# Optimization experiments

Measured on AMD Instinct MI355X. Metric: run time of the kernel, lower is better.

## Reference

```python
import jax, jax.numpy as jnp
import numpy as np


def setup_inputs() -> dict:
    key = jax.random.key(0)
    ks = jax.random.split(key, 6)
    B, C, H, W = 8, 512, 64, 64
    s = 1.0 / np.sqrt(C)
    return {
        "x": jax.random.normal(ks[0], (B, C, H, W), dtype=jnp.float32),
        "w_phi": jax.random.normal(ks[1], (C, C), dtype=jnp.float32) * s,
        "w_theta": jax.random.normal(ks[2], (C, C), dtype=jnp.float32) * s,
        "w_g": jax.random.normal(ks[3], (C, C), dtype=jnp.float32) * s,
        "w_mask": jax.random.normal(ks[4], (C, C), dtype=jnp.float32) * s,
        "gamma": jax.random.normal(ks[5], (1,), dtype=jnp.float32) * 0.1,
    }


def reference(x, w_phi, w_theta, w_g, w_mask, gamma):
    b, c, h, w = x.shape
    n = h * w
    xf = x.reshape(b, c, n)  # flatten spatial: [b, c, n]
    # 1x1 convs (bias=False) are channel-mixing GEMMs
    phi = jnp.einsum("oc,bcn->bon", w_phi, xf)    # [b, c, n]
    theta = jnp.einsum("oc,bcn->bon", w_theta, xf)  # [b, c, n]
    g = jnp.einsum("oc,bcn->bon", w_g, xf)        # [b, c, n]
    # channel-channel attention (unscaled), softmax over last dim
    attn = jax.nn.softmax(jnp.einsum("bcn,bdn->bcd", phi, theta), axis=-1)  # [b, c, c]
    y = jnp.einsum("bcd,bdn->bcn", attn, g)  # [b, c, n]
    # faithful to torch: permute(0,2,1).contiguous().view(b, c, h, w)
    y = jnp.transpose(y, (0, 2, 1)).reshape(b, c, h, w)
    mask = jnp.einsum("oc,bchw->bohw", w_mask, y)
    return mask * gamma[0] + x
```

## Files before the change

kernel.cpp:

```cpp
#include <hip/hip_runtime.h>
#include <hip/hip_bf16.h>

constexpr int BATCH = 8;
constexpr int C = 512;
constexpr int HW = 4096;
constexpr long CN = (long)C * HW;
constexpr long CC = (long)C * C;

typedef __attribute__((ext_vector_type(8))) short short8;
typedef __attribute__((ext_vector_type(4))) short bf16x4;
typedef __attribute__((ext_vector_type(4))) float f32x4;

__device__ __forceinline__ void gload16(const void* g, void* l) {
  __builtin_amdgcn_global_load_lds(
      (const __attribute__((address_space(1))) void*)g,
      (__attribute__((address_space(3))) void*)l, 16, 0, 0);
}

__device__ __forceinline__ void hilo(float v, __hip_bfloat16& h, __hip_bfloat16& l) {
  h = __float2bfloat16(v);
  l = __float2bfloat16(v - __bfloat162float(h));
}
__device__ __forceinline__ short bfs(float v) {
  __hip_bfloat16 h = __float2bfloat16(v);
  return *(short*)&h;
}

__device__ __forceinline__ int cidx32(int r, int ch) {
  return ((r >> 1) * 8 + ((((r & 1) << 2) | ch) ^ ((r >> 1) & 7))) * 8;
}
__device__ __forceinline__ void sdec32(int s, int& r, int& ch) {
  int R = s >> 3, q = s & 7, v = q ^ (R & 7);
  r = (R << 1) | (v >> 2);
  ch = v & 3;
}

#define WAIT_VM(n) asm volatile("s_waitcnt vmcnt(" #n ")" ::: "memory")

__global__ __launch_bounds__(256) void convx_k(
    const float* __restrict__ x, __hip_bfloat16* __restrict__ xhi,
    __hip_bfloat16* __restrict__ xt) {
  const int b = blockIdx.z;
  const int n0 = blockIdx.x * 64, c0 = blockIdx.y * 64;
  const float* xb = x + (long)b * CN;
  __shared__ short t[64 * 65];
  const int tid = threadIdx.x;
#pragma unroll
  for (int it = 0; it < 2; ++it) {
    int slot = it * 256 + tid;
    int r = slot >> 3, cc = (slot & 7) * 8;
    const float* src = xb + (long)(c0 + r) * HW + n0 + cc;
    f32x4 v0 = *(const f32x4*)src, v1 = *(const f32x4*)(src + 4);
    short8 hh;
#pragma unroll
    for (int e = 0; e < 4; ++e) {
      hh[e] = bfs(v0[e]);
      hh[4 + e] = bfs(v1[e]);
    }
    long idx = (long)b * CN + (long)(c0 + r) * HW + n0 + cc;
    *(short8*)((short*)xhi + idx) = hh;
#pragma unroll
    for (int e = 0; e < 8; ++e) t[r * 65 + cc + e] = hh[e];
  }
  __syncthreads();
#pragma unroll
  for (int it = 0; it < 2; ++it) {
    int slot = it * 256 + tid;
    int r = slot >> 3, cc = (slot & 7) * 8;
    short8 o;
#pragma unroll
    for (int e = 0; e < 8; ++e) o[e] = t[(cc + e) * 65 + r];
    *(short8*)((short*)xt + (long)b * CN + (long)(n0 + r) * C + c0 + cc) = o;
  }
}

__global__ __launch_bounds__(256) void wprep_k(
    const float* __restrict__ wphi, const float* __restrict__ wtheta,
    const float* __restrict__ wg, const float* __restrict__ wmask,
    __hip_bfloat16* __restrict__ wph, __hip_bfloat16* __restrict__ wpl,
    __hip_bfloat16* __restrict__ wth, __hip_bfloat16* __restrict__ wtl,
    __hip_bfloat16* __restrict__ wgT, __hip_bfloat16* __restrict__ wm16) {
  const int z = blockIdx.z;
  const int r0 = blockIdx.y * 64, c0 = blockIdx.x * 64;
  const int tid = threadIdx.x;
  if (z == 2) {
    __shared__ __hip_bfloat16 t[64][65];
#pragma unroll
    for (int i = 0; i < 16; ++i) {
      int e = i * 256 + tid;
      int r = e >> 6, c = e & 63;
      t[r][c] = __float2bfloat16(wg[(long)(r0 + r) * C + c0 + c]);
    }
    __syncthreads();
#pragma unroll
    for (int i = 0; i < 16; ++i) {
      int e = i * 256 + tid;
      int r = e >> 6, c = e & 63;
      wgT[(long)(c0 + r) * C + r0 + c] = t[c][r];
    }
  } else {
#pragma unroll
    for (int i = 0; i < 16; ++i) {
      int e = i * 256 + tid;
      int r = e >> 6, c = e & 63;
      long idx = (long)(r0 + r) * C + c0 + c;
      if (z == 0) {
        __hip_bfloat16 h, l;
        hilo(wphi[idx], h, l);
        wph[idx] = h; wpl[idx] = l;
      } else if (z == 1) {
        __hip_bfloat16 h, l;
        hilo(wtheta[idx], h, l);
        wth[idx] = h; wtl[idx] = l;
      } else {
        wm16[idx] = __float2bfloat16(wmask[idx]);
      }
    }
  }
}

__global__ __launch_bounds__(256) void gram_k(
    const __hip_bfloat16* __restrict__ xhi, float* __restrict__ gpart) {
  const int b = blockIdx.z;
  const int ks = blockIdx.y;
  int i = 0, rem0 = blockIdx.x;
  while (rem0 >= 4 - i) { rem0 -= 4 - i; ++i; }
  const int j = i + rem0;
  const int m0 = i * 128, n0 = j * 128;

  const short* X = (const short*)(xhi + (long)b * CN);
  __shared__ short lds[4 * 8192];
  const int tid = threadIdx.x, w = tid >> 6, lane = tid & 63;

  f32x4 acc[4][4] = {};
  const int wr = (w >> 1) * 64, wc = (w & 1) * 64;
  const int kbeg = ks * 1024;
  constexpr int NST = 32;

  auto STAGE = [&](int buf, int k0) {
    short* lb = lds + buf * 8192;
#pragma unroll
    for (int it = 0; it < 4; ++it) {
      int s = (w & 1) * 256 + it * 64 + lane;
      int r, ch;
      sdec32(s, r, ch);
      int gr = (w < 2) ? (m0 + r) : (n0 + r);
      gload16(X + (long)gr * HW + k0 + ch * 8, lb + (w >> 1) * 4096 + s * 8);
    }
  };

  const int chf = lane >> 4, rl = lane & 15;
  int aoff[4], boff[4];
#pragma unroll
  for (int mi = 0; mi < 4; ++mi) aoff[mi] = cidx32(wr + mi * 16 + rl, chf);
#pragma unroll
  for (int ni = 0; ni < 4; ++ni) boff[ni] = 4096 + cidx32(wc + ni * 16 + rl, chf);

  STAGE(0, kbeg);
  STAGE(1, kbeg + 32);
  STAGE(2, kbeg + 64);

#pragma unroll
  for (int t = 0; t < NST; ++t) {
    if (t + 3 < NST) STAGE((t + 3) & 3, kbeg + (t + 3) * 32);
    const int rm = NST - 1 - t;
    if (rm >= 3) WAIT_VM(12);
    else if (rm == 2) WAIT_VM(8);
    else if (rm == 1) WAIT_VM(4);
    else WAIT_VM(0);
    __builtin_amdgcn_s_barrier();
    const short* lb = lds + (t & 3) * 8192;
    short8 af[4], bfr[4];
#pragma unroll
    for (int mi = 0; mi < 4; ++mi) af[mi] = *(const short8*)(lb + aoff[mi]);
#pragma unroll
    for (int ni = 0; ni < 4; ++ni) bfr[ni] = *(const short8*)(lb + boff[ni]);
#pragma unroll
    for (int mi = 0; mi < 4; ++mi)
#pragma unroll
      for (int ni = 0; ni < 4; ++ni)
        acc[mi][ni] = __builtin_amdgcn_mfma_f32_16x16x32_bf16(af[mi], bfr[ni], acc[mi][ni], 0, 0, 0);
    __builtin_amdgcn_s_barrier();
  }

  float* P = gpart + ((((long)b * 10 + blockIdx.x) * 4 + ks) << 14);
#pragma unroll
  for (int mi = 0; mi < 4; ++mi)
#pragma unroll
    for (int ni = 0; ni < 4; ++ni)
#pragma unroll
      for (int rr = 0; rr < 4; ++rr) {
        int row = wr + mi * 16 + (lane >> 4) * 4 + rr;
        int col = wc + ni * 16 + (lane & 15);
        P[row * 128 + col] = acc[mi][ni][rr];
      }
}

__global__ __launch_bounds__(256) void gred_k(
    const float* __restrict__ gpart, __hip_bfloat16* __restrict__ gh,
    __hip_bfloat16* __restrict__ gl) {
  const int b = blockIdx.z;
  const int half = blockIdx.y;
  int i = 0, rem = blockIdx.x;
  while (rem >= 4 - i) { rem -= 4 - i; ++i; }
  const int j = i + rem;
  const int m0 = i * 128, n0 = j * 128;
  const float* P = gpart + (((long)b * 10 + blockIdx.x) << 16) + half * 8192;
  __shared__ float T[128][65];
  const int tid = threadIdx.x;
  const long dbase = (long)b * CC;

#pragma unroll
  for (int q = 0; q < 8; ++q) {
    int e = q * 1024 + tid * 4;
    int r = e >> 7, c = e & 127;
    f32x4 s = {};
#pragma unroll
    for (int ks = 0; ks < 4; ++ks) s += *(const f32x4*)(P + (ks << 14) + e);
    bf16x4 hh, ll;
#pragma unroll
    for (int u = 0; u < 4; ++u) {
      __hip_bfloat16 h, l;
      hilo(s[u], h, l);
      hh[u] = *(short*)&h;
      ll[u] = *(short*)&l;
      T[c + u][r] = s[u];
    }
    long idx = dbase + (long)(m0 + half * 64 + r) * 512 + n0 + c;
    *(bf16x4*)((short*)gh + idx) = hh;
    *(bf16x4*)((short*)gl + idx) = ll;
  }
  if (i != j) {
    __syncthreads();
#pragma unroll
    for (int q = 0; q < 8; ++q) {
      int e = q * 1024 + tid * 4;
      int rp = e >> 6, cp = e & 63;
      bf16x4 hh, ll;
#pragma unroll
      for (int u = 0; u < 4; ++u) {
        __hip_bfloat16 h, l;
        hilo(T[rp][cp + u], h, l);
        hh[u] = *(short*)&h;
        ll[u] = *(short*)&l;
      }
      long idx = dbase + (long)(n0 + rp) * 512 + m0 + half * 64 + cp;
      *(bf16x4*)((short*)gh + idx) = hh;
      *(bf16x4*)((short*)gl + idx) = ll;
    }
  }
}

template <int AH, int BH, int EPI>
__global__ __launch_bounds__(256) void nt_small(
    const __hip_bfloat16* __restrict__ Ah_, const __hip_bfloat16* __restrict__ Al_,
    const __hip_bfloat16* __restrict__ Bh_, const __hip_bfloat16* __restrict__ Bl_,
    long aStr, long bStr, void* __restrict__ out1, void* __restrict__ out2) {
  const int b = blockIdx.z;
  const int m0 = blockIdx.y * 64, n0 = blockIdx.x * 64;
  const short* Ahp = (const short*)(Ah_ + (long)b * aStr);
  const short* Alp = AH ? (const short*)(Al_ + (long)b * aStr) : nullptr;
  const short* Bhp = (const short*)(Bh_ + (long)b * bStr);
  const short* Blp = BH ? (const short*)(Bl_ + (long)b * bStr) : nullptr;
  constexpr int PAN = (AH && BH) ? 4 : 2;
  __shared__ short lds[2 * PAN * 4096];
  const int tid = threadIdx.x, w = tid >> 6, lane = tid & 63;

  f32x4 acc[2][2] = {};
  const int wr = (w >> 1) * 32, wc = (w & 1) * 32;

  auto STAGE = [&](int buf, int k0) {
    short* lb = lds + buf * PAN * 4096;
    if constexpr (AH && BH) {
      const short* src = (w == 0) ? Ahp : (w == 1) ? Alp : (w == 2) ? Bhp : Blp;
      const int rowbase = (w & 2) ? n0 : m0;
      short* lt = lb + w * 4096;
#pragma unroll
      for (int it = 0; it < 8; ++it) {
        int slot = it * 64 + lane;
        int r = slot >> 3, p = slot & 7, c = p ^ (r & 7);
        gload16(src + (long)(rowbase + r) * 512 + k0 + c * 8, lt + slot * 8);
      }
    } else {
      const short* src = (w < 2) ? Ahp : Bhp;
      const int rowbase = (w < 2) ? m0 : n0;
      short* lt = lb + (w >> 1) * 4096;
#pragma unroll
      for (int it = 0; it < 4; ++it) {
        int slot = (w & 1) * 256 + it * 64 + lane;
        int r = slot >> 3, p = slot & 7, c = p ^ (r & 7);
        gload16(src + (long)(rowbase + r) * 512 + k0 + c * 8, lt + slot * 8);
      }
    }
  };

  STAGE(0, 0);
  asm volatile("s_waitcnt vmcnt(0)" ::: "memory");
  __builtin_amdgcn_s_barrier();

  for (int t = 0; t < 8; ++t) {
    if (t < 7) STAGE((t + 1) & 1, (t + 1) * 64);
    const short* lb = lds + (t & 1) * PAN * 4096;
#pragma unroll
    for (int kh = 0; kh < 2; ++kh) {
      short8 ah[2], al[2], bh[2], bl[2];
      const int ch = kh * 4 + (lane >> 4);
#pragma unroll
      for (int mi = 0; mi < 2; ++mi) {
        int r = wr + mi * 16 + (lane & 15);
        int off = (r * 8 + (ch ^ (r & 7))) * 8;
        ah[mi] = *(const short8*)(lb + off);
        if constexpr (AH) al[mi] = *(const short8*)(lb + 4096 + off);
      }
#pragma unroll
      for (int ni = 0; ni < 2; ++ni) {
        int r = wc + ni * 16 + (lane & 15);
        int off = (r * 8 + (ch ^ (r & 7))) * 8;
        bh[ni] = *(const short8*)(lb + ((AH && BH) ? 8192 : 4096) + off);
        if constexpr (BH) bl[ni] = *(const short8*)(lb + 12288 + off);
      }
#pragma unroll
      for (int mi = 0; mi < 2; ++mi)
#pragma unroll
        for (int ni = 0; ni < 2; ++ni) {
          acc[mi][ni] = __builtin_amdgcn_mfma_f32_16x16x32_bf16(ah[mi], bh[ni], acc[mi][ni], 0, 0, 0);
          if constexpr (BH)
            acc[mi][ni] = __builtin_amdgcn_mfma_f32_16x16x32_bf16(ah[mi], bl[ni], acc[mi][ni], 0, 0, 0);
          if constexpr (AH)
            acc[mi][ni] = __builtin_amdgcn_mfma_f32_16x16x32_bf16(al[mi], bh[ni], acc[mi][ni], 0, 0, 0);
        }
    }
    asm volatile("s_waitcnt vmcnt(0)" ::: "memory");
    __builtin_amdgcn_s_barrier();
  }

#pragma unroll
  for (int mi = 0; mi < 2; ++mi)
#pragma unroll
    for (int ni = 0; ni < 2; ++ni)
#pragma unroll
      for (int rr = 0; rr < 4; ++rr) {
        int row = m0 + wr + mi * 16 + (lane >> 4) * 4 + rr;
        int col = n0 + wc + ni * 16 + (lane & 15);
        long idx = (long)b * CC + (long)row * 512 + col;
        float v = acc[mi][ni][rr];
        if constexpr (EPI == 0) {
          __hip_bfloat16 h, l;
          hilo(v, h, l);
          ((__hip_bfloat16*)out1)[idx] = h;
          ((__hip_bfloat16*)out2)[idx] = l;
        } else if constexpr (EPI == 1) {
          ((float*)out1)[idx] = v;
        } else {
          ((__hip_bfloat16*)out1)[idx] = __float2bfloat16(v);
        }
      }
}

__global__ __launch_bounds__(256) void softmax_k(const float* __restrict__ a,
                                                 __hip_bfloat16* __restrict__ o) {
  const float* row = a + (long)blockIdx.x * 512;
  __hip_bfloat16* orow = o + (long)blockIdx.x * 512;
  const int t = threadIdx.x;
  float v0 = row[t], v1 = row[t + 256];
  __shared__ float sm[256];
  sm[t] = fmaxf(v0, v1);
  __syncthreads();
  for (int s = 128; s > 0; s >>= 1) {
    if (t < s) sm[t] = fmaxf(sm[t], sm[t + s]);
    __syncthreads();
  }
  float mx = sm[0];
  __syncthreads();
  float e0 = expf(v0 - mx), e1 = expf(v1 - mx);
  sm[t] = e0 + e1;
  __syncthreads();
  for (int s = 128; s > 0; s >>= 1) {
    if (t < s) sm[t] += sm[t + s];
    __syncthreads();
  }
  float inv = 1.0f / sm[0];
  orow[t] = __float2bfloat16(e0 * inv);
  orow[t + 256] = __float2bfloat16(e1 * inv);
}

template <int MODE>
__global__ __launch_bounds__(256) void big_k(
    const __hip_bfloat16* __restrict__ Aw, const __hip_bfloat16* __restrict__ Bm,
    void* __restrict__ Cout, const float* __restrict__ x,
    const float* __restrict__ gammaPtr, long aStride) {
  const int b = blockIdx.z;
  const int lin = ((blockIdx.x & 7) << 4) | (blockIdx.x >> 3);
  const int m0 = (lin & 3) * 128;
  const int n0 = (lin >> 2) * 128;
  const short* A = (const short*)(Aw + (long)b * aStride);
  const short* B = (const short*)(Bm + (long)b * CN);
  __shared__ short lds[4 * 8192];
  const int tid = threadIdx.x, w = tid >> 6, lane = tid & 63;

  f32x4 acc[4][4] = {};
  const int wr = (w >> 1) * 64, wc = (w & 1) * 64;
  constexpr int NST = 16;

  auto STAGE = [&](int buf, int k0) {
    short* lb = lds + buf * 8192;
#pragma unroll
    for (int it = 0; it < 4; ++it) {
      int s = (w & 1) * 256 + it * 64 + lane;
      int r, ch;
      sdec32(s, r, ch);
      if (w < 2) {
        gload16(A + (long)(m0 + r) * 512 + k0 + ch * 8, lb + s * 8);
      } else {
        int gr = (MODE == 0) ? (n0 + (r & 15) * 8 + (r >> 4)) : (n0 + r);
        gload16(B + (long)gr * 512 + k0 + ch * 8, lb + 4096 + s * 8);
      }
    }
  };

  const int chf = lane >> 4, rl = lane & 15;
  int aoff[4], boff[4];
#pragma unroll
  for (int mi = 0; mi < 4; ++mi) aoff[mi] = cidx32(wr + mi * 16 + rl, chf);
#pragma unroll
  for (int ni = 0; ni < 4; ++ni) boff[ni] = 4096 + cidx32(wc + ni * 16 + rl, chf);

  STAGE(0, 0);
  STAGE(1, 32);
  STAGE(2, 64);

#pragma unroll
  for (int t = 0; t < NST; ++t) {
    if (t + 3 < NST) STAGE((t + 3) & 3, (t + 3) * 32);
    const int rm = NST - 1 - t;
    if (rm >= 3) WAIT_VM(12);
    else if (rm == 2) WAIT_VM(8);
    else if (rm == 1) WAIT_VM(4);
    else WAIT_VM(0);
    __builtin_amdgcn_s_barrier();
    const short* lb = lds + (t & 3) * 8192;
    short8 af[4], bfr[4];
#pragma unroll
    for (int mi = 0; mi < 4; ++mi) af[mi] = *(const short8*)(lb + aoff[mi]);
#pragma unroll
    for (int ni = 0; ni < 4; ++ni) bfr[ni] = *(const short8*)(lb + boff[ni]);
#pragma unroll
    for (int mi = 0; mi < 4; ++mi)
#pragma unroll
      for (int ni = 0; ni < 4; ++ni)
        acc[mi][ni] = __builtin_amdgcn_mfma_f32_16x16x32_bf16(af[mi], bfr[ni], acc[mi][ni], 0, 0, 0);
    __builtin_amdgcn_s_barrier();
  }

  if (MODE == 0) {
    __hip_bfloat16* yv = (__hip_bfloat16*)Cout + (long)b * CN;
    const int u = lane & 15;
#pragma unroll
    for (int mi = 0; mi < 4; ++mi)
#pragma unroll
      for (int ni = 0; ni < 4; ++ni) {
        int t = (wc >> 4) + ni;
        long base = ((long)(t * 512 + m0 + wr + mi * 16 + (lane >> 4) * 4)) * 512 +
                    (n0 >> 3) + u;
#pragma unroll
        for (int r = 0; r < 4; ++r)
          yv[base + (long)r * 512] = __float2bfloat16(acc[mi][ni][r]);
      }
  } else {
    float* outp = (float*)Cout + (long)b * CN;
    const float* xb = x + (long)b * CN;
    const float g0 = gammaPtr[0];
#pragma unroll
    for (int mi = 0; mi < 4; ++mi)
#pragma unroll
      for (int ni = 0; ni < 4; ++ni)
#pragma unroll
        for (int r = 0; r < 4; ++r) {
          long idx = (long)(m0 + wr + mi * 16 + (lane >> 4) * 4 + r) * HW +
                     n0 + wc + ni * 16 + (lane & 15);
          outp[idx] = g0 * acc[mi][ni][r] + xb[idx];
        }
  }
}

extern "C" void kernel_launch(void* const* d_in, const int* in_sizes, int n_in,
                              void* d_out, int out_size, void* d_ws, size_t ws_size,
                              hipStream_t stream) {
  const float* x       = (const float*)d_in[0];
  const float* w_phi   = (const float*)d_in[1];
  const float* w_theta = (const float*)d_in[2];
  const float* w_g     = (const float*)d_in[3];
  const float* w_mask  = (const float*)d_in[4];
  const float* gamma   = (const float*)d_in[5];
  float* out = (float*)d_out;

  __hip_bfloat16* xhi = (__hip_bfloat16*)d_ws;
  __hip_bfloat16* xt  = xhi + BATCH * CN;
  __hip_bfloat16* gh  = xt + BATCH * CN;
  __hip_bfloat16* gl  = gh + BATCH * CC;
  __hip_bfloat16* t1h = gl + BATCH * CC;
  __hip_bfloat16* t1l = t1h + BATCH * CC;
  __hip_bfloat16* wph = t1l + BATCH * CC;
  __hip_bfloat16* wpl = wph + CC;
  __hip_bfloat16* wth = wpl + CC;
  __hip_bfloat16* wtl = wth + CC;
  __hip_bfloat16* wgT = wtl + CC;
  __hip_bfloat16* wm16 = wgT + CC;
  float* gpart = (float*)(wm16 + CC);
  float* logits           = (float*)gh;
  __hip_bfloat16* attn16  = t1h;
  __hip_bfloat16* mb16    = t1l;
  __hip_bfloat16* yvT     = xhi;

  convx_k<<<dim3(64, 8, BATCH), 256, 0, stream>>>(x, xhi, xt);
  wprep_k<<<dim3(8, 8, 4), 256, 0, stream>>>(w_phi, w_theta, w_g, w_mask,
                                             wph, wpl, wth, wtl, wgT, wm16);
  gram_k<<<dim3(10, 4, BATCH), 256, 0, stream>>>(xhi, gpart);
  gred_k<<<dim3(10, 2, BATCH), 256, 0, stream>>>(gpart, gh, gl);
  nt_small<1, 1, 0><<<dim3(8, 8, BATCH), 256, 0, stream>>>(
      wph, wpl, gh, gl, 0, CC, t1h, t1l);
  nt_small<1, 1, 1><<<dim3(8, 8, BATCH), 256, 0, stream>>>(
      t1h, t1l, wth, wtl, CC, 0, logits, nullptr);
  softmax_k<<<dim3(BATCH * C), dim3(256), 0, stream>>>(logits, attn16);
  nt_small<0, 0, 2><<<dim3(8, 8, BATCH), 256, 0, stream>>>(
      attn16, nullptr, wgT, nullptr, CC, 0, mb16, nullptr);
  big_k<0><<<dim3(128, 1, BATCH), 256, 0, stream>>>(mb16, xt, yvT, nullptr, nullptr, CC);
  big_k<1><<<dim3(128, 1, BATCH), 256, 0, stream>>>(wm16, yvT, out, x, gamma, 0);
}
```

Before: 270.4 us.

## Fuse small attention GEMM chain and softmax into one per-row-block kernel

Replaces the three nt_small launches and the separate softmax kernel with one chain_k kernel. Each block computes 32 rows of W_phi·G, keeps the intermediate in LDS as hi/lo bf16, multiplies by W_theta, does the softmax in registers with cross-wave reductions, then multiplies by W_g^T and writes mb16. This removes global round trips for t1, the logits and attn, plus three launches. The cost is a grid of only 128 blocks reading B operands straight from global memory without LDS staging, which may leave the GPU underused. It also remaps gram_k block indices so the batch index varies fastest across consecutive blocks.

```diff
diff --git a/kernel.cpp b/kernel.cpp
--- a/kernel.cpp
+++ b/kernel.cpp
@@ -121,9 +121,12 @@
 
 __global__ __launch_bounds__(256) void gram_k(
     const __hip_bfloat16* __restrict__ xhi, float* __restrict__ gpart) {
-  const int b = blockIdx.z;
-  const int ks = blockIdx.y;
-  int i = 0, rem0 = blockIdx.x;
+  const int f = blockIdx.x + 10 * (blockIdx.y + 4 * blockIdx.z);
+  const int b = f & 7;
+  const int rdec = f >> 3;
+  const int ks = rdec / 10;
+  const int tile = rdec % 10;
+  int i = 0, rem0 = tile;
   while (rem0 >= 4 - i) { rem0 -= 4 - i; ++i; }
   const int j = i + rem0;
   const int m0 = i * 128, n0 = j * 128;
@@ -145,7 +148,8 @@
       int r, ch;
       sdec32(s, r, ch);
       int gr = (w < 2) ? (m0 + r) : (n0 + r);
-      gload16(X + (long)gr * HW + k0 + ch * 8, lb + (w >> 1) * 4096 + s * 8);
+      gload16(X + (long)gr * HW + k0 + ch * 8, lds + (buf * 8192 + (w >> 1) * 4096 + s * 8));
+      (void)lb;
     }
   };
 
@@ -183,7 +187,7 @@
     __builtin_amdgcn_s_barrier();
   }
 
-  float* P = gpart + ((((long)b * 10 + blockIdx.x) * 4 + ks) << 14);
+  float* P = gpart + ((((long)b * 10 + tile) * 4 + ks) << 14);
 #pragma unroll
   for (int mi = 0; mi < 4; ++mi)
 #pragma unroll
@@ -251,137 +255,208 @@
   }
 }
 
-template <int AH, int BH, int EPI>
-__global__ __launch_bounds__(256) void nt_small(
-    const __hip_bfloat16* __restrict__ Ah_, const __hip_bfloat16* __restrict__ Al_,
-    const __hip_bfloat16* __restrict__ Bh_, const __hip_bfloat16* __restrict__ Bl_,
-    long aStr, long bStr, void* __restrict__ out1, void* __restrict__ out2) {
-  const int b = blockIdx.z;
-  const int m0 = blockIdx.y * 64, n0 = blockIdx.x * 64;
-  const short* Ahp = (const short*)(Ah_ + (long)b * aStr);
-  const short* Alp = AH ? (const short*)(Al_ + (long)b * aStr) : nullptr;
-  const short* Bhp = (const short*)(Bh_ + (long)b * bStr);
-  const short* Blp = BH ? (const short*)(Bl_ + (long)b * bStr) : nullptr;
-  constexpr int PAN = (AH && BH) ? 4 : 2;
-  __shared__ short lds[2 * PAN * 4096];
+__global__ __launch_bounds__(256) void chain_k(
+    const __hip_bfloat16* __restrict__ wph_, const __hip_bfloat16* __restrict__ wpl_,
+    const __hip_bfloat16* __restrict__ gh_, const __hip_bfloat16* __restrict__ gl_,
+    const __hip_bfloat16* __restrict__ wth_, const __hip_bfloat16* __restrict__ wtl_,
+    const __hip_bfloat16* __restrict__ wgT_, __hip_bfloat16* __restrict__ mb16) {
+  const int f = blockIdx.x + 16 * blockIdx.z;
+  const int b = f & 7;
+  const int m0 = (f >> 3) * 32;
+
+  const short* Ah = (const short*)wph_;
+  const short* Al = (const short*)wpl_;
+  const short* Gh = (const short*)(gh_ + (long)b * CC);
+  const short* Gl = (const short*)(gl_ + (long)b * CC);
+  const short* Th = (const short*)wth_;
+  const short* Tl = (const short*)wtl_;
+  const short* Wg = (const short*)wgT_;
+
+  __shared__ short t1h[32 * 512];
+  __shared__ short t1l[32 * 512];
+  __shared__ short at[32 * 512];
+  __shared__ float red[4][32];
+  __shared__ float rowv[32];
+
   const int tid = threadIdx.x, w = tid >> 6, lane = tid & 63;
-
-  f32x4 acc[2][2] = {};
-  const int wr = (w >> 1) * 32, wc = (w & 1) * 32;
-
-  auto STAGE = [&](int buf, int k0) {
-    short* lb = lds + buf * PAN * 4096;
-    if constexpr (AH && BH) {
-      const short* src = (w == 0) ? Ahp : (w == 1) ? Alp : (w == 2) ? Bhp : Blp;
-      const int rowbase = (w & 2) ? n0 : m0;
-      short* lt = lb + w * 4096;
-#pragma unroll
-      for (int it = 0; it < 8; ++it) {
-        int slot = it * 64 + lane;
-        int r = slot >> 3, p = slot & 7, c = p ^ (r & 7);
-        gload16(src + (long)(rowbase + r) * 512 + k0 + c * 8, lt + slot * 8);
-      }
-    } else {
-      const short* src = (w < 2) ? Ahp : Bhp;
-      const int rowbase = (w < 2) ? m0 : n0;
-      short* lt = lb + (w >> 1) * 4096;
-#pragma unroll
-      for (int it = 0; it < 4; ++it) {
-        int slot = (w & 1) * 256 + it * 64 + lane;
-        int r = slot >> 3, p = slot & 7, c = p ^ (r & 7);
-        gload16(src + (long)(rowbase + r) * 512 + k0 + c * 8, lt + slot * 8);
-      }
-    }
-  };
-
-  STAGE(0, 0);
-  asm volatile("s_waitcnt vmcnt(0)" ::: "memory");
-  __builtin_amdgcn_s_barrier();
-
-  for (int t = 0; t < 8; ++t) {
-    if (t < 7) STAGE((t + 1) & 1, (t + 1) * 64);
-    const short* lb = lds + (t & 1) * PAN * 4096;
-#pragma unroll
-    for (int kh = 0; kh < 2; ++kh) {
-      short8 ah[2], al[2], bh[2], bl[2];
-      const int ch = kh * 4 + (lane >> 4);
+  const int ch = lane >> 4, u = lane & 15;
+  const int nbase = w * 128;
+
+  f32x4 acc[2][8];
+
+#pragma unroll
+  for (int mi = 0; mi < 2; ++mi)
+#pragma unroll
+    for (int ni = 0; ni < 8; ++ni) acc[mi][ni] = (f32x4){0.f, 0.f, 0.f, 0.f};
+
+#pragma unroll 2
+  for (int kb = 0; kb < 512; kb += 32) {
+    short8 ah[2], al[2];
+#pragma unroll
+    for (int mi = 0; mi < 2; ++mi) {
+      int ao = (m0 + mi * 16 + u) * 512 + kb + ch * 8;
+      ah[mi] = *(const short8*)(Ah + ao);
+      al[mi] = *(const short8*)(Al + ao);
+    }
+#pragma unroll
+    for (int ni = 0; ni < 8; ++ni) {
+      int bo = (nbase + ni * 16 + u) * 512 + kb + ch * 8;
+      short8 bh = *(const short8*)(Gh + bo);
+      short8 bl = *(const short8*)(Gl + bo);
 #pragma unroll
       for (int mi = 0; mi < 2; ++mi) {
-        int r = wr + mi * 16 + (lane & 15);
-        int off = (r * 8 + (ch ^ (r & 7))) * 8;
-        ah[mi] = *(const short8*)(lb + off);
-        if constexpr (AH) al[mi] = *(const short8*)(lb + 4096 + off);
-      }
-#pragma unroll
-      for (int ni = 0; ni < 2; ++ni) {
-        int r = wc + ni * 16 + (lane & 15);
-        int off = (r * 8 + (ch ^ (r & 7))) * 8;
-        bh[ni] = *(const short8*)(lb + ((AH && BH) ? 8192 : 4096) + off);
-        if constexpr (BH) bl[ni] = *(const short8*)(lb + 12288 + off);
-      }
+        acc[mi][ni] = __builtin_amdgcn_mfma_f32_16x16x32_bf16(ah[mi], bh, acc[mi][ni], 0, 0, 0);
+        acc[mi][ni] = __builtin_amdgcn_mfma_f32_16x16x32_bf16(ah[mi], bl, acc[mi][ni], 0, 0, 0);
+        acc[mi][ni] = __builtin_amdgcn_mfma_f32_16x16x32_bf16(al[mi], bh, acc[mi][ni], 0, 0, 0);
+      }
+    }
+  }
+
+#pragma unroll
+  for (int mi = 0; mi < 2; ++mi)
+#pragma unroll
+    for (int ni = 0; ni < 8; ++ni)
+#pragma unroll
+      for (int rr = 0; rr < 4; ++rr) {
+        int m = mi * 16 + ch * 4 + rr;
+        int c = nbase + ni * 16 + u;
+        int addr = m * 512 + ((((c >> 3) ^ (m & 7)) << 3) | (c & 7));
+        __hip_bfloat16 h, l;
+        hilo(acc[mi][ni][rr], h, l);
+        t1h[addr] = *(short*)&h;
+        t1l[addr] = *(short*)&l;
+      }
+  __syncthreads();
+
+#pragma unroll
+  for (int mi = 0; mi < 2; ++mi)
+#pragma unroll
+    for (int ni = 0; ni < 8; ++ni) acc[mi][ni] = (f32x4){0.f, 0.f, 0.f, 0.f};
+
+#pragma unroll 2
+  for (int kb = 0; kb < 512; kb += 32) {
+    short8 ah[2], al[2];
+#pragma unroll
+    for (int mi = 0; mi < 2; ++mi) {
+      int m = mi * 16 + u;
+      int p = (kb >> 3) + ch;
+      int off = (m * 64 + (p ^ (m & 7))) * 8;
+      ah[mi] = *(const short8*)(t1h + off);
+      al[mi] = *(const short8*)(t1l + off);
+    }
+#pragma unroll
+    for (int ni = 0; ni < 8; ++ni) {
+      int bo = (nbase + ni * 16 + u) * 512 + kb + ch * 8;
+      short8 bh = *(const short8*)(Th + bo);
+      short8 bl = *(const short8*)(Tl + bo);
+#pragma unroll
+      for (int mi = 0; mi < 2; ++mi) {
+        acc[mi][ni] = __builtin_amdgcn_mfma_f32_16x16x32_bf16(ah[mi], bh, acc[mi][ni], 0, 0, 0);
+        acc[mi][ni] = __builtin_amdgcn_mfma_f32_16x16x32_bf16(ah[mi], bl, acc[mi][ni], 0, 0, 0);
+        acc[mi][ni] = __builtin_amdgcn_mfma_f32_16x16x32_bf16(al[mi], bh, acc[mi][ni], 0, 0, 0);
+      }
+    }
+  }
+
+  float rm[2][4];
+#pragma unroll
+  for (int mi = 0; mi < 2; ++mi)
+#pragma unroll
+    for (int rr = 0; rr < 4; ++rr) {
+      float v = acc[mi][0][rr];
+#pragma unroll
+      for (int ni = 1; ni < 8; ++ni) v = fmaxf(v, acc[mi][ni][rr]);
+#pragma unroll
+      for (int s = 1; s < 16; s <<= 1) v = fmaxf(v, __shfl_xor(v, s));
+      rm[mi][rr] = v;
+    }
+  if (u == 0)
+#pragma unroll
+    for (int mi = 0; mi < 2; ++mi)
+#pragma unroll
+      for (int rr = 0; rr < 4; ++rr) red[w][mi * 16 + ch * 4 + rr] = rm[mi][rr];
+  __syncthreads();
+  if (tid < 32)
+    rowv[tid] = fmaxf(fmaxf(red[0][tid], red[1][tid]), fmaxf(red[2][tid], red[3][tid]));
+  __syncthreads();
+
+  float rs[2][4];
+#pragma unroll
+  for (int mi = 0; mi < 2; ++mi)
+#pragma unroll
+    for (int rr = 0; rr < 4; ++rr) {
+      float M = rowv[mi * 16 + ch * 4 + rr];
+      float s = 0.f;
+#pragma unroll
+      for (int ni = 0; ni < 8; ++ni) {
+        float e = expf(acc[mi][ni][rr] - M);
+        acc[mi][ni][rr] = e;
+        s += e;
+      }
+#pragma unroll
+      for (int t = 1; t < 16; t <<= 1) s += __shfl_xor(s, t);
+      rs[mi][rr] = s;
+    }
+  if (u == 0)
+#pragma unroll
+    for (int mi = 0; mi < 2; ++mi)
+#pragma unroll
+      for (int rr = 0; rr < 4; ++rr) red[w][mi * 16 + ch * 4 + rr] = rs[mi][rr];
+  __syncthreads();
+  if (tid < 32)
+    rowv[tid] = 1.0f / (red[0][tid] + red[1][tid] + red[2][tid] + red[3][tid]);
+  __syncthreads();
+
+#pragma unroll
+  for (int mi = 0; mi < 2; ++mi)
+#pragma unroll
+    for (int rr = 0; rr < 4; ++rr) {
+      int m = mi * 16 + ch * 4 + rr;
+      float inv = rowv[m];
+#pragma unroll
+      for (int ni = 0; ni < 8; ++ni) {
+        int c = nbase + ni * 16 + u;
+        int addr = m * 512 + ((((c >> 3) ^ (m & 7)) << 3) | (c & 7));
+        at[addr] = bfs(acc[mi][ni][rr] * inv);
+      }
+    }
+  __syncthreads();
+
+#pragma unroll
+  for (int mi = 0; mi < 2; ++mi)
+#pragma unroll
+    for (int ni = 0; ni < 8; ++ni) acc[mi][ni] = (f32x4){0.f, 0.f, 0.f, 0.f};
+
+#pragma unroll 2
+  for (int kb = 0; kb < 512; kb += 32) {
+    short8 ah[2];
+#pragma unroll
+    for (int mi = 0; mi < 2; ++mi) {
+      int m = mi * 16 + u;
+      int p = (kb >> 3) + ch;
+      ah[mi] = *(const short8*)(at + (m * 64 + (p ^ (m & 7))) * 8);
+    }
+#pragma unroll
+    for (int ni = 0; ni < 8; ++ni) {
+      int bo = (nbase + ni * 16 + u) * 512 + kb + ch * 8;
+      short8 bg = *(const short8*)(Wg + bo);
 #pragma unroll
       for (int mi = 0; mi < 2; ++mi)
-#pragma unroll
-        for (int ni = 0; ni < 2; ++ni) {
-          acc[mi][ni] = __builtin_amdgcn_mfma_f32_16x16x32_bf16(ah[mi], bh[ni], acc[mi][ni], 0, 0, 0);
-          if constexpr (BH)
-            acc[mi][ni] = __builtin_amdgcn_mfma_f32_16x16x32_bf16(ah[mi], bl[ni], acc[mi][ni], 0, 0, 0);
-          if constexpr (AH)
-            acc[mi][ni] = __builtin_amdgcn_mfma_f32_16x16x32_bf16(al[mi], bh[ni], acc[mi][ni], 0, 0, 0);
-        }
-    }
-    asm volatile("s_waitcnt vmcnt(0)" ::: "memory");
-    __builtin_amdgcn_s_barrier();
-  }
-
-#pragma unroll
-  for (int mi = 0; mi < 2; ++mi)
-#pragma unroll
-    for (int ni = 0; ni < 2; ++ni)
+        acc[mi][ni] = __builtin_amdgcn_mfma_f32_16x16x32_bf16(ah[mi], bg, acc[mi][ni], 0, 0, 0);
+    }
+  }
+
+  short* outp = (short*)mb16 + (long)b * CC;
+#pragma unroll
+  for (int mi = 0; mi < 2; ++mi)
+#pragma unroll
+    for (int ni = 0; ni < 8; ++ni)
 #pragma unroll
       for (int rr = 0; rr < 4; ++rr) {
-        int row = m0 + wr + mi * 16 + (lane >> 4) * 4 + rr;
-        int col = n0 + wc + ni * 16 + (lane & 15);
-        long idx = (long)b * CC + (long)row * 512 + col;
-        float v = acc[mi][ni][rr];
-        if constexpr (EPI == 0) {
-          __hip_bfloat16 h, l;
-          hilo(v, h, l);
-          ((__hip_bfloat16*)out1)[idx] = h;
-          ((__hip_bfloat16*)out2)[idx] = l;
-        } else if constexpr (EPI == 1) {
-          ((float*)out1)[idx] = v;
-        } else {
-          ((__hip_bfloat16*)out1)[idx] = __float2bfloat16(v);
-        }
-      }
-}
-
-__global__ __launch_bounds__(256) void softmax_k(const float* __restrict__ a,
-                                                 __hip_bfloat16* __restrict__ o) {
-  const float* row = a + (long)blockIdx.x * 512;
-  __hip_bfloat16* orow = o + (long)blockIdx.x * 512;
-  const int t = threadIdx.x;
-  float v0 = row[t], v1 = row[t + 256];
-  __shared__ float sm[256];
-  sm[t] = fmaxf(v0, v1);
-  __syncthreads();
-  for (int s = 128; s > 0; s >>= 1) {
-    if (t < s) sm[t] = fmaxf(sm[t], sm[t + s]);
-    __syncthreads();
-  }
-  float mx = sm[0];
-  __syncthreads();
-  float e0 = expf(v0 - mx), e1 = expf(v1 - mx);
-  sm[t] = e0 + e1;
-  __syncthreads();
-  for (int s = 128; s > 0; s >>= 1) {
-    if (t < s) sm[t] += sm[t + s];
-    __syncthreads();
-  }
-  float inv = 1.0f / sm[0];
-  orow[t] = __float2bfloat16(e0 * inv);
-  orow[t + 256] = __float2bfloat16(e1 * inv);
+        int row = m0 + mi * 16 + ch * 4 + rr;
+        int col = nbase + ni * 16 + u;
+        outp[row * 512 + col] = bfs(acc[mi][ni][rr]);
+      }
 }
 
 template <int MODE>
@@ -507,23 +582,17 @@
   __hip_bfloat16* wgT = wtl + CC;
   __hip_bfloat16* wm16 = wgT + CC;
   float* gpart = (float*)(wm16 + CC);
-  float* logits           = (float*)gh;
-  __hip_bfloat16* attn16  = t1h;
   __hip_bfloat16* mb16    = t1l;
   __hip_bfloat16* yvT     = xhi;
+  (void)t1h;
 
   convx_k<<<dim3(64, 8, BATCH), 256, 0, stream>>>(x, xhi, xt);
   wprep_k<<<dim3(8, 8, 4), 256, 0, stream>>>(w_phi, w_theta, w_g, w_mask,
                                              wph, wpl, wth, wtl, wgT, wm16);
   gram_k<<<dim3(10, 4, BATCH), 256, 0, stream>>>(xhi, gpart);
   gred_k<<<dim3(10, 2, BATCH), 256, 0, stream>>>(gpart, gh, gl);
-  nt_small<1, 1, 0><<<dim3(8, 8, BATCH), 256, 0, stream>>>(
-      wph, wpl, gh, gl, 0, CC, t1h, t1l);
-  nt_small<1, 1, 1><<<dim3(8, 8, BATCH), 256, 0, stream>>>(
-      t1h, t1l, wth, wtl, CC, 0, logits, nullptr);
-  softmax_k<<<dim3(BATCH * C), dim3(256), 0, stream>>>(logits, attn16);
-  nt_small<0, 0, 2><<<dim3(8, 8, BATCH), 256, 0, stream>>>(
-      attn16, nullptr, wgT, nullptr, CC, 0, mb16, nullptr);
+  chain_k<<<dim3(16, 1, BATCH), 256, 0, stream>>>(wph, wpl, gh, gl,
+                                                  wth, wtl, wgT, mb16);
   big_k<0><<<dim3(128, 1, BATCH), 256, 0, stream>>>(mb16, xt, yvT, nullptr, nullptr, CC);
   big_k<1><<<dim3(128, 1, BATCH), 256, 0, stream>>>(wm16, yvT, out, x, gamma, 0);
 }
```

After: 328.7 us. 21.6% more time.

## Interleave batch in block index for small kernels and use wave-per-row softmax

Applied to the files above, without the earlier changes.

Block indices for gram, gram-reduce and the small NT GEMMs are flattened so batch is the fastest-varying index. Consecutive workgroups then come from different batches, which changes how work spreads across XCDs and caches. The softmax is rewritten so each wavefront handles one row using vector loads and shuffle reductions, replacing a shared-memory tree with many barriers. The remapping may lower L2 locality within a batch on some chiplets.

```diff
diff --git a/kernel.cpp b/kernel.cpp
--- a/kernel.cpp
+++ b/kernel.cpp
@@ -121,9 +121,12 @@
 
 __global__ __launch_bounds__(256) void gram_k(
     const __hip_bfloat16* __restrict__ xhi, float* __restrict__ gpart) {
-  const int b = blockIdx.z;
-  const int ks = blockIdx.y;
-  int i = 0, rem0 = blockIdx.x;
+  const int f = blockIdx.x + 10 * (blockIdx.y + 4 * blockIdx.z);
+  const int b = f & 7;
+  const int rdec = f >> 3;
+  const int ks = rdec / 10;
+  const int tile = rdec % 10;
+  int i = 0, rem0 = tile;
   while (rem0 >= 4 - i) { rem0 -= 4 - i; ++i; }
   const int j = i + rem0;
   const int m0 = i * 128, n0 = j * 128;
@@ -138,14 +141,13 @@
   constexpr int NST = 32;
 
   auto STAGE = [&](int buf, int k0) {
-    short* lb = lds + buf * 8192;
 #pragma unroll
     for (int it = 0; it < 4; ++it) {
       int s = (w & 1) * 256 + it * 64 + lane;
       int r, ch;
       sdec32(s, r, ch);
       int gr = (w < 2) ? (m0 + r) : (n0 + r);
-      gload16(X + (long)gr * HW + k0 + ch * 8, lb + (w >> 1) * 4096 + s * 8);
+      gload16(X + (long)gr * HW + k0 + ch * 8, lds + (buf * 8192 + (w >> 1) * 4096 + s * 8));
     }
   };
 
@@ -183,7 +185,7 @@
     __builtin_amdgcn_s_barrier();
   }
 
-  float* P = gpart + ((((long)b * 10 + blockIdx.x) * 4 + ks) << 14);
+  float* P = gpart + ((((long)b * 10 + tile) * 4 + ks) << 14);
 #pragma unroll
   for (int mi = 0; mi < 4; ++mi)
 #pragma unroll
@@ -199,13 +201,16 @@
 __global__ __launch_bounds__(256) void gred_k(
     const float* __restrict__ gpart, __hip_bfloat16* __restrict__ gh,
     __hip_bfloat16* __restrict__ gl) {
-  const int b = blockIdx.z;
-  const int half = blockIdx.y;
-  int i = 0, rem = blockIdx.x;
+  const int id = blockIdx.x;
+  const int b = id & 7;
+  const int t2 = id >> 3;
+  const int tile = t2 % 10;
+  const int half = t2 / 10;
+  int i = 0, rem = tile;
   while (rem >= 4 - i) { rem -= 4 - i; ++i; }
   const int j = i + rem;
   const int m0 = i * 128, n0 = j * 128;
-  const float* P = gpart + (((long)b * 10 + blockIdx.x) << 16) + half * 8192;
+  const float* P = gpart + (((long)b * 10 + tile) << 16) + half * 8192;
   __shared__ float T[128][65];
   const int tid = threadIdx.x;
   const long dbase = (long)b * CC;
@@ -256,8 +261,10 @@
     const __hip_bfloat16* __restrict__ Ah_, const __hip_bfloat16* __restrict__ Al_,
     const __hip_bfloat16* __restrict__ Bh_, const __hip_bfloat16* __restrict__ Bl_,
     long aStr, long bStr, void* __restrict__ out1, void* __restrict__ out2) {
-  const int b = blockIdx.z;
-  const int m0 = blockIdx.y * 64, n0 = blockIdx.x * 64;
+  const int id = blockIdx.x;
+  const int b = id & 7;
+  const int rest = id >> 3;
+  const int m0 = (rest >> 3) * 64, n0 = (rest & 7) * 64;
   const short* Ahp = (const short*)(Ah_ + (long)b * aStr);
   const short* Alp = AH ? (const short*)(Al_ + (long)b * aStr) : nullptr;
   const short* Bhp = (const short*)(Bh_ + (long)b * bStr);
@@ -359,29 +366,30 @@
 
 __global__ __launch_bounds__(256) void softmax_k(const float* __restrict__ a,
                                                  __hip_bfloat16* __restrict__ o) {
-  const float* row = a + (long)blockIdx.x * 512;
-  __hip_bfloat16* orow = o + (long)blockIdx.x * 512;
-  const int t = threadIdx.x;
-  float v0 = row[t], v1 = row[t + 256];
-  __shared__ float sm[256];
-  sm[t] = fmaxf(v0, v1);
-  __syncthreads();
-  for (int s = 128; s > 0; s >>= 1) {
-    if (t < s) sm[t] = fmaxf(sm[t], sm[t + s]);
-    __syncthreads();
-  }
-  float mx = sm[0];
-  __syncthreads();
-  float e0 = expf(v0 - mx), e1 = expf(v1 - mx);
-  sm[t] = e0 + e1;
-  __syncthreads();
-  for (int s = 128; s > 0; s >>= 1) {
-    if (t < s) sm[t] += sm[t + s];
-    __syncthreads();
-  }
-  float inv = 1.0f / sm[0];
-  orow[t] = __float2bfloat16(e0 * inv);
-  orow[t + 256] = __float2bfloat16(e1 * inv);
+  const int id = blockIdx.x;
+  const int b = id & 7, rg = id >> 3;
+  const int w = threadIdx.x >> 6, lane = threadIdx.x & 63;
+  const long row = (long)b * 512 + rg * 4 + w;
+  const float* rp = a + row * 512 + lane * 8;
+  f32x4 v0 = *(const f32x4*)rp, v1 = *(const f32x4*)(rp + 4);
+  float mx = fmaxf(fmaxf(fmaxf(v0[0], v0[1]), fmaxf(v0[2], v0[3])),
+                   fmaxf(fmaxf(v1[0], v1[1]), fmaxf(v1[2], v1[3])));
+#pragma unroll
+  for (int s = 1; s < 64; s <<= 1) mx = fmaxf(mx, __shfl_xor(mx, s));
+  float e[8];
+#pragma unroll
+  for (int k = 0; k < 4; ++k) {
+    e[k] = expf(v0[k] - mx);
+    e[4 + k] = expf(v1[k] - mx);
+  }
+  float sum = ((e[0] + e[1]) + (e[2] + e[3])) + ((e[4] + e[5]) + (e[6] + e[7]));
+#pragma unroll
+  for (int s = 1; s < 64; s <<= 1) sum += __shfl_xor(sum, s);
+  const float inv = 1.0f / sum;
+  short8 o8;
+#pragma unroll
+  for (int k = 0; k < 8; ++k) o8[k] = bfs(e[k] * inv);
+  *(short8*)((short*)o + row * 512 + lane * 8) = o8;
 }
 
 template <int MODE>
@@ -516,13 +524,13 @@
   wprep_k<<<dim3(8, 8, 4), 256, 0, stream>>>(w_phi, w_theta, w_g, w_mask,
                                              wph, wpl, wth, wtl, wgT, wm16);
   gram_k<<<dim3(10, 4, BATCH), 256, 0, stream>>>(xhi, gpart);
-  gred_k<<<dim3(10, 2, BATCH), 256, 0, stream>>>(gpart, gh, gl);
-  nt_small<1, 1, 0><<<dim3(8, 8, BATCH), 256, 0, stream>>>(
+  gred_k<<<dim3(160, 1, 1), 256, 0, stream>>>(gpart, gh, gl);
+  nt_small<1, 1, 0><<<dim3(512, 1, 1), 256, 0, stream>>>(
       wph, wpl, gh, gl, 0, CC, t1h, t1l);
-  nt_small<1, 1, 1><<<dim3(8, 8, BATCH), 256, 0, stream>>>(
+  nt_small<1, 1, 1><<<dim3(512, 1, 1), 256, 0, stream>>>(
       t1h, t1l, wth, wtl, CC, 0, logits, nullptr);
-  softmax_k<<<dim3(BATCH * C), dim3(256), 0, stream>>>(logits, attn16);
-  nt_small<0, 0, 2><<<dim3(8, 8, BATCH), 256, 0, stream>>>(
+  softmax_k<<<dim3(1024, 1, 1), dim3(256), 0, stream>>>(logits, attn16);
+  nt_small<0, 0, 2><<<dim3(512, 1, 1), 256, 0, stream>>>(
       attn16, nullptr, wgT, nullptr, CC, 0, mb16, nullptr);
   big_k<0><<<dim3(128, 1, BATCH), 256, 0, stream>>>(mb16, xt, yvT, nullptr, nullptr, CC);
   big_k<1><<<dim3(128, 1, BATCH), 256, 0, stream>>>(wm16, yvT, out, x, gamma, 0);
```

After: 255.6 us. -5.5%, faster.
